# Kernel optimization log

Hardware: AMD Instinct MI355X
Metric: run time of the kernel (lower is better)

## Reference

```python
import jax, jax.numpy as jnp
import numpy as np

LN_EPS = 1e-5  # torch nn.LayerNorm default


def setup_inputs() -> dict:
    key = jax.random.key(0)
    ks = jax.random.split(key, 5)
    B, N, K, H, D = 1, 16384, 16, 4, 32
    q = jax.random.normal(ks[0], (B, N, H, D), dtype=jnp.float32)
    k_neigh = jax.random.normal(ks[1], (B, N, K, H, D), dtype=jnp.float32)
    v_neigh = jax.random.normal(ks[2], (B, N, K, H, D), dtype=jnp.float32)
    geo_f = jax.random.normal(ks[3], (B, N, K, D), dtype=jnp.float32)
    W = jax.random.normal(ks[4], (D, D), dtype=jnp.float32) * (1.0 / np.sqrt(D))
    b = jnp.zeros((D,), dtype=jnp.float32)
    ln_gamma = jnp.ones((D,), dtype=jnp.float32)
    ln_beta = jnp.zeros((D,), dtype=jnp.float32)
    return {"q": q, "k_neigh": k_neigh, "v_neigh": v_neigh, "geo_f": geo_f,
            "W": W, "b": b, "ln_gamma": ln_gamma, "ln_beta": ln_beta}


def reference(q, k_neigh, v_neigh, geo_f, W, b, ln_gamma, ln_beta):
    # q: [B,N,H,D], k_neigh/v_neigh: [B,N,K,H,D], geo_f: [B,N,K,D]
    scale = q.shape[-1] ** (-0.5)
    # broadcasted edge tensor [B,N,K,H,D]
    w = (q[:, :, None, :, :] - k_neigh + geo_f[:, :, :, None, :]) / scale
    # Linear(hdim,hdim) + ReLU + LayerNorm(hdim)
    w = jnp.einsum('bnkhd,ed->bnkhe', w, W) + b
    w = jax.nn.relu(w)
    mu = jnp.mean(w, axis=-1, keepdims=True)
    var = jnp.mean(jnp.square(w - mu), axis=-1, keepdims=True)
    w = (w - mu) * jax.lax.rsqrt(var + LN_EPS) * ln_gamma + ln_beta
    # subtract detached per-neighbor max (shift-invariant for softmax)
    w = w - jax.lax.stop_gradient(jnp.max(w, axis=2, keepdims=True))
    attn = jax.nn.softmax(w, axis=2)  # softmax over K neighbors
    # dropout p=0.0 -> identity
    out = jnp.sum(attn * v_neigh, axis=2)  # [B,N,H,D]
    return out
```

## Files before the change

kernel.cpp:

```cpp
#include <hip/hip_runtime.h>
#include <math.h>

constexpr int KNB = 16;
constexpr int HH  = 4;
constexpr int DD  = 32;

typedef __attribute__((ext_vector_type(4))) float f32x4;
typedef __attribute__((ext_vector_type(8))) short bf16x8;
typedef __attribute__((ext_vector_type(4))) short s16x4;

__device__ __forceinline__ unsigned short f2bf(float f) {
    union { float f; unsigned u; } v; v.f = f;
    const unsigned r = v.u + 0x7fffu + ((v.u >> 16) & 1u);
    return (unsigned short)(r >> 16);
}
__device__ __forceinline__ float bf2f(unsigned short b) {
    union { unsigned u; float f; } v; v.u = ((unsigned)b) << 16; return v.f;
}

__global__ __launch_bounds__(256) void geoneigh_mfma(
    const float* __restrict__ q, const float* __restrict__ kn,
    const float* __restrict__ vn, const float* __restrict__ geo,
    const float* __restrict__ W, const float* __restrict__ bvec,
    const float* __restrict__ gamma, const float* __restrict__ beta,
    float* __restrict__ out, int BN)
{
    __shared__ short wt[4][2][2][16][32];

    const int l  = threadIdx.x & 63;
    const int wv = threadIdx.x >> 6;
    const int gw = blockIdx.x * 4 + wv;
    const int n  = gw >> 1;
    if (n >= BN) return;
    const int h0 = (gw & 1) * 2;

    const int lm = l & 15;
    const int lg = l >> 4;
    const int r8 = l >> 3;
    const int dq = l & 7;

    bf16x8 Wh[2], Wl[2];
    #pragma unroll
    for (int t = 0; t < 2; ++t) {
        const float* wr = &W[(t * 16 + lm) * DD + lg * 8];
        const float4 a = *(const float4*)wr;
        const float4 b = *(const float4*)(wr + 4);
        const float wf[8] = {a.x, a.y, a.z, a.w, b.x, b.y, b.z, b.w};
        #pragma unroll
        for (int j = 0; j < 8; ++j) {
            const unsigned short h = f2bf(wf[j]);
            Wh[t][j] = (short)h;
            Wl[t][j] = (short)f2bf(wf[j] - bf2f(h));
        }
    }
    float bias[2], gam[2], bet[2];
    #pragma unroll
    for (int t = 0; t < 2; ++t) {
        bias[t] = bvec[lm + 16 * t];
        gam[t]  = gamma[lm + 16 * t];
        bet[t]  = beta[lm + 16 * t];
    }

    const float SC = 5.656854249492381f;

    float4 g4[2], q4[2], k4[2][2];
    #pragma unroll
    for (int j = 0; j < 2; ++j)
        g4[j] = *(const float4*)&geo[((size_t)n * KNB + r8 + 8 * j) * DD + dq * 4];
    #pragma unroll
    for (int u = 0; u < 2; ++u) {
        const int h = h0 + u;
        q4[u] = *(const float4*)&q[((size_t)n * HH + h) * DD + dq * 4];
        #pragma unroll
        for (int j = 0; j < 2; ++j)
            k4[u][j] = *(const float4*)&kn[(((size_t)n * KNB + r8 + 8 * j) * HH + h) * DD + dq * 4];
    }

    #pragma unroll
    for (int u = 0; u < 2; ++u) {
        #pragma unroll
        for (int j = 0; j < 2; ++j) {
            const int row = r8 + 8 * j;
            const float w0 = (q4[u].x - k4[u][j].x + g4[j].x) * SC;
            const float w1 = (q4[u].y - k4[u][j].y + g4[j].y) * SC;
            const float w2 = (q4[u].z - k4[u][j].z + g4[j].z) * SC;
            const float w3 = (q4[u].w - k4[u][j].w + g4[j].w) * SC;
            const unsigned short a0 = f2bf(w0), a1 = f2bf(w1), a2 = f2bf(w2), a3 = f2bf(w3);
            const s16x4 hi = {(short)a0, (short)a1, (short)a2, (short)a3};
            const s16x4 lo = {(short)f2bf(w0 - bf2f(a0)), (short)f2bf(w1 - bf2f(a1)),
                              (short)f2bf(w2 - bf2f(a2)), (short)f2bf(w3 - bf2f(a3))};
            *(s16x4*)&wt[wv][u][0][row][dq * 4] = hi;
            *(s16x4*)&wt[wv][u][1][row][dq * 4] = lo;
        }
    }
    asm volatile("" ::: "memory");

    bf16x8 Ah[2], Al[2];
    #pragma unroll
    for (int u = 0; u < 2; ++u) {
        Ah[u] = *(const bf16x8*)&wt[wv][u][0][lm][lg * 8];
        Al[u] = *(const bf16x8*)&wt[wv][u][1][lm][lg * 8];
    }

    float vreg[2][2][4];
    #pragma unroll
    for (int u = 0; u < 2; ++u)
        #pragma unroll
        for (int t = 0; t < 2; ++t)
            #pragma unroll
            for (int r = 0; r < 4; ++r)
                vreg[u][t][r] =
                    vn[(((size_t)n * KNB + lg * 4 + r) * HH + h0 + u) * DD + lm + 16 * t];

    f32x4 acc[2][2];
    #pragma unroll
    for (int u = 0; u < 2; ++u)
        #pragma unroll
        for (int t = 0; t < 2; ++t) {
            f32x4 c = {0.f, 0.f, 0.f, 0.f};
            c = __builtin_amdgcn_mfma_f32_16x16x32_bf16(Ah[u], Wh[t], c, 0, 0, 0);
            c = __builtin_amdgcn_mfma_f32_16x16x32_bf16(Ah[u], Wl[t], c, 0, 0, 0);
            c = __builtin_amdgcn_mfma_f32_16x16x32_bf16(Al[u], Wh[t], c, 0, 0, 0);
            acc[u][t] = c;
        }

    #pragma unroll
    for (int u = 0; u < 2; ++u) {
        float x[2][4], t1[4], t2[4];
        #pragma unroll
        for (int t = 0; t < 2; ++t)
            #pragma unroll
            for (int r = 0; r < 4; ++r)
                x[t][r] = fmaxf(acc[u][t][r] + bias[t], 0.f);
        #pragma unroll
        for (int r = 0; r < 4; ++r) {
            t1[r] = x[0][r] + x[1][r];
            t2[r] = x[0][r] * x[0][r] + x[1][r] * x[1][r];
        }
        #pragma unroll
        for (int m = 1; m <= 8; m <<= 1) {
            #pragma unroll
            for (int r = 0; r < 4; ++r) {
                t1[r] += __shfl_xor(t1[r], m);
                t2[r] += __shfl_xor(t2[r], m);
            }
        }
        float z[2][4];
        #pragma unroll
        for (int r = 0; r < 4; ++r) {
            const float mu  = t1[r] * 0.03125f;
            const float var = fmaxf(t2[r] * 0.03125f - mu * mu, 0.f);
            const float inv = rsqrtf(var + 1e-5f);
            #pragma unroll
            for (int t = 0; t < 2; ++t)
                z[t][r] = (x[t][r] - mu) * inv * gam[t] + bet[t];
        }
        float S[2], o[2];
        #pragma unroll
        for (int t = 0; t < 2; ++t) {
            float mx = fmaxf(fmaxf(z[t][0], z[t][1]), fmaxf(z[t][2], z[t][3]));
            mx = fmaxf(mx, __shfl_xor(mx, 16));
            mx = fmaxf(mx, __shfl_xor(mx, 32));
            float s = 0.f, oo = 0.f;
            #pragma unroll
            for (int r = 0; r < 4; ++r) {
                const float p = __expf(z[t][r] - mx);
                s += p;
                oo = fmaf(p, vreg[u][t][r], oo);
            }
            s  += __shfl_xor(s, 16);
            s  += __shfl_xor(s, 32);
            oo += __shfl_xor(oo, 16);
            oo += __shfl_xor(oo, 32);
            S[t] = s; o[t] = oo;
        }
        if (l < 32) {
            const int   sel = lg & 1;
            const float os  = sel ? o[1] : o[0];
            const float ss  = sel ? S[1] : S[0];
            out[((size_t)n * HH + h0 + u) * DD + l] = __fdividef(os, ss);
        }
    }
}

extern "C" void kernel_launch(void* const* d_in, const int* in_sizes, int n_in,
                              void* d_out, int out_size, void* d_ws, size_t ws_size,
                              hipStream_t stream) {
    const float* q   = (const float*)d_in[0];
    const float* kn  = (const float*)d_in[1];
    const float* vn  = (const float*)d_in[2];
    const float* geo = (const float*)d_in[3];
    const float* W   = (const float*)d_in[4];
    const float* b   = (const float*)d_in[5];
    const float* gam = (const float*)d_in[6];
    const float* bet = (const float*)d_in[7];
    float* out = (float*)d_out;

    const int BN     = in_sizes[0] / (HH * DD);
    const int waves  = BN * 2;
    const int blocks = (waves + 3) / 4;

    hipLaunchKernelGGL(geoneigh_mfma, dim3(blocks), dim3(256), 0, stream,
                       q, kn, vn, geo, W, b, gam, bet, out, BN);
}
```

Measured before the change: 66.90 us.

## Load MFMA A-fragments directly from global memory, skipping the LDS staging

Each lane now loads q, k and geo in the exact layout of the MFMA A-operand (row = neighbor, 8 contiguous d values). This removes the shared-memory write/read round trip used before to transpose the edge tensor. It also folds the 1/scale factor into W, seeds the accumulator with the bias, uses packed hardware bf16 conversions, and merges the two per-head output stores into one full-wave store. The direct loads are 32-byte per lane with a different coalescing pattern, and each q row is now read by 16 lanes.

```diff
diff --git a/kernel.cpp b/kernel.cpp
--- a/kernel.cpp
+++ b/kernel.cpp
@@ -1,4 +1,5 @@
 #include <hip/hip_runtime.h>
+#include <hip/hip_bf16.h>
 #include <math.h>
 
 constexpr int KNB = 16;
@@ -7,50 +8,51 @@
 
 typedef __attribute__((ext_vector_type(4))) float f32x4;
 typedef __attribute__((ext_vector_type(8))) short bf16x8;
-typedef __attribute__((ext_vector_type(4))) short s16x4;
-
-__device__ __forceinline__ unsigned short f2bf(float f) {
-    union { float f; unsigned u; } v; v.f = f;
-    const unsigned r = v.u + 0x7fffu + ((v.u >> 16) & 1u);
-    return (unsigned short)(r >> 16);
-}
-__device__ __forceinline__ float bf2f(unsigned short b) {
-    union { unsigned u; float f; } v; v.u = ((unsigned)b) << 16; return v.f;
-}
-
-__global__ __launch_bounds__(256) void geoneigh_mfma(
+
+union BFRAG { bf16x8 v; unsigned u[4]; };
+
+__device__ __forceinline__ unsigned pk_bf16(float a, float b) {
+    union { __hip_bfloat162 b2; unsigned u; } r;
+    r.b2 = __float22bfloat162_rn(make_float2(a, b));
+    return r.u;
+}
+__device__ __forceinline__ float2 unpk_bf16(unsigned u) {
+    union { unsigned u; __hip_bfloat162 b2; } r; r.u = u;
+    return make_float2(__bfloat162float(r.b2.x), __bfloat162float(r.b2.y));
+}
+
+__global__ __launch_bounds__(256) void geoneigh_mfma2(
     const float* __restrict__ q, const float* __restrict__ kn,
     const float* __restrict__ vn, const float* __restrict__ geo,
     const float* __restrict__ W, const float* __restrict__ bvec,
     const float* __restrict__ gamma, const float* __restrict__ beta,
     float* __restrict__ out, int BN)
 {
-    __shared__ short wt[4][2][2][16][32];
-
     const int l  = threadIdx.x & 63;
-    const int wv = threadIdx.x >> 6;
-    const int gw = blockIdx.x * 4 + wv;
+    const int gw = blockIdx.x * 4 + (threadIdx.x >> 6);
     const int n  = gw >> 1;
     if (n >= BN) return;
     const int h0 = (gw & 1) * 2;
 
     const int lm = l & 15;
     const int lg = l >> 4;
-    const int r8 = l >> 3;
-    const int dq = l & 7;
-
-    bf16x8 Wh[2], Wl[2];
+
+    const float SC = 5.656854249492381f;
+
+    BFRAG Wh[2], Wl[2];
     #pragma unroll
     for (int t = 0; t < 2; ++t) {
         const float* wr = &W[(t * 16 + lm) * DD + lg * 8];
-        const float4 a = *(const float4*)wr;
-        const float4 b = *(const float4*)(wr + 4);
-        const float wf[8] = {a.x, a.y, a.z, a.w, b.x, b.y, b.z, b.w};
-        #pragma unroll
-        for (int j = 0; j < 8; ++j) {
-            const unsigned short h = f2bf(wf[j]);
-            Wh[t][j] = (short)h;
-            Wl[t][j] = (short)f2bf(wf[j] - bf2f(h));
+        const float4 wa = *(const float4*)wr;
+        const float4 wb = *(const float4*)(wr + 4);
+        float wf[8] = {wa.x * SC, wa.y * SC, wa.z * SC, wa.w * SC,
+                       wb.x * SC, wb.y * SC, wb.z * SC, wb.w * SC};
+        #pragma unroll
+        for (int p = 0; p < 4; ++p) {
+            const unsigned h = pk_bf16(wf[2 * p], wf[2 * p + 1]);
+            const float2 hr = unpk_bf16(h);
+            Wh[t].u[p] = h;
+            Wl[t].u[p] = pk_bf16(wf[2 * p] - hr.x, wf[2 * p + 1] - hr.y);
         }
     }
     float bias[2], gam[2], bet[2];
@@ -61,69 +63,64 @@
         bet[t]  = beta[lm + 16 * t];
     }
 
-    const float SC = 5.656854249492381f;
-
-    float4 g4[2], q4[2], k4[2][2];
-    #pragma unroll
-    for (int j = 0; j < 2; ++j)
-        g4[j] = *(const float4*)&geo[((size_t)n * KNB + r8 + 8 * j) * DD + dq * 4];
+    const size_t nn = (size_t)n;
+    const float* kb = kn  + ((nn * KNB + lm) * HH + h0) * DD + lg * 8;
+    const float* gb = geo + (nn * KNB + lm) * DD + lg * 8;
+    const float* qb = q   + (nn * HH + h0) * DD + lg * 8;
+
+    const float4 gf0 = *(const float4*)gb;
+    const float4 gf1 = *(const float4*)(gb + 4);
+    float4 kf[2][2], qf[2][2];
     #pragma unroll
     for (int u = 0; u < 2; ++u) {
-        const int h = h0 + u;
-        q4[u] = *(const float4*)&q[((size_t)n * HH + h) * DD + dq * 4];
-        #pragma unroll
-        for (int j = 0; j < 2; ++j)
-            k4[u][j] = *(const float4*)&kn[(((size_t)n * KNB + r8 + 8 * j) * HH + h) * DD + dq * 4];
-    }
-
+        kf[u][0] = *(const float4*)(kb + u * DD);
+        kf[u][1] = *(const float4*)(kb + u * DD + 4);
+        qf[u][0] = *(const float4*)(qb + u * DD);
+        qf[u][1] = *(const float4*)(qb + u * DD + 4);
+    }
+
+    const float* vb = vn + ((nn * KNB + lg * 4) * HH + h0) * DD + lm;
+    float vreg[2][2][4];
+    #pragma unroll
+    for (int u = 0; u < 2; ++u)
+        #pragma unroll
+        for (int t = 0; t < 2; ++t)
+            #pragma unroll
+            for (int r = 0; r < 4; ++r)
+                vreg[u][t][r] = vb[((size_t)r * HH + u) * DD + 16 * t];
+
+    f32x4 acc[2][2];
     #pragma unroll
     for (int u = 0; u < 2; ++u) {
-        #pragma unroll
-        for (int j = 0; j < 2; ++j) {
-            const int row = r8 + 8 * j;
-            const float w0 = (q4[u].x - k4[u][j].x + g4[j].x) * SC;
-            const float w1 = (q4[u].y - k4[u][j].y + g4[j].y) * SC;
-            const float w2 = (q4[u].z - k4[u][j].z + g4[j].z) * SC;
-            const float w3 = (q4[u].w - k4[u][j].w + g4[j].w) * SC;
-            const unsigned short a0 = f2bf(w0), a1 = f2bf(w1), a2 = f2bf(w2), a3 = f2bf(w3);
-            const s16x4 hi = {(short)a0, (short)a1, (short)a2, (short)a3};
-            const s16x4 lo = {(short)f2bf(w0 - bf2f(a0)), (short)f2bf(w1 - bf2f(a1)),
-                              (short)f2bf(w2 - bf2f(a2)), (short)f2bf(w3 - bf2f(a3))};
-            *(s16x4*)&wt[wv][u][0][row][dq * 4] = hi;
-            *(s16x4*)&wt[wv][u][1][row][dq * 4] = lo;
-        }
-    }
-    asm volatile("" ::: "memory");
-
-    bf16x8 Ah[2], Al[2];
-    #pragma unroll
-    for (int u = 0; u < 2; ++u) {
-        Ah[u] = *(const bf16x8*)&wt[wv][u][0][lm][lg * 8];
-        Al[u] = *(const bf16x8*)&wt[wv][u][1][lm][lg * 8];
-    }
-
-    float vreg[2][2][4];
-    #pragma unroll
-    for (int u = 0; u < 2; ++u)
-        #pragma unroll
-        for (int t = 0; t < 2; ++t)
-            #pragma unroll
-            for (int r = 0; r < 4; ++r)
-                vreg[u][t][r] =
-                    vn[(((size_t)n * KNB + lg * 4 + r) * HH + h0 + u) * DD + lm + 16 * t];
-
-    f32x4 acc[2][2];
-    #pragma unroll
-    for (int u = 0; u < 2; ++u)
+        float wv[8];
+        #pragma unroll
+        for (int p = 0; p < 2; ++p) {
+            const float4 kq = kf[u][p], qq = qf[u][p];
+            const float4 gg = p ? gf1 : gf0;
+            wv[4 * p + 0] = qq.x - kq.x + gg.x;
+            wv[4 * p + 1] = qq.y - kq.y + gg.y;
+            wv[4 * p + 2] = qq.z - kq.z + gg.z;
+            wv[4 * p + 3] = qq.w - kq.w + gg.w;
+        }
+        BFRAG Ah, Al;
+        #pragma unroll
+        for (int p = 0; p < 4; ++p) {
+            const unsigned h = pk_bf16(wv[2 * p], wv[2 * p + 1]);
+            const float2 hr = unpk_bf16(h);
+            Ah.u[p] = h;
+            Al.u[p] = pk_bf16(wv[2 * p] - hr.x, wv[2 * p + 1] - hr.y);
+        }
         #pragma unroll
         for (int t = 0; t < 2; ++t) {
-            f32x4 c = {0.f, 0.f, 0.f, 0.f};
-            c = __builtin_amdgcn_mfma_f32_16x16x32_bf16(Ah[u], Wh[t], c, 0, 0, 0);
-            c = __builtin_amdgcn_mfma_f32_16x16x32_bf16(Ah[u], Wl[t], c, 0, 0, 0);
-            c = __builtin_amdgcn_mfma_f32_16x16x32_bf16(Al[u], Wh[t], c, 0, 0, 0);
+            f32x4 c = {bias[t], bias[t], bias[t], bias[t]};
+            c = __builtin_amdgcn_mfma_f32_16x16x32_bf16(Ah.v, Wh[t].v, c, 0, 0, 0);
+            c = __builtin_amdgcn_mfma_f32_16x16x32_bf16(Ah.v, Wl[t].v, c, 0, 0, 0);
+            c = __builtin_amdgcn_mfma_f32_16x16x32_bf16(Al.v, Wh[t].v, c, 0, 0, 0);
             acc[u][t] = c;
         }
-
+    }
+
+    float outv[2], sumv[2];
     #pragma unroll
     for (int u = 0; u < 2; ++u) {
         float x[2][4], t1[4], t2[4];
@@ -131,7 +128,7 @@
         for (int t = 0; t < 2; ++t)
             #pragma unroll
             for (int r = 0; r < 4; ++r)
-                x[t][r] = fmaxf(acc[u][t][r] + bias[t], 0.f);
+                x[t][r] = fmaxf(acc[u][t][r], 0.f);
         #pragma unroll
         for (int r = 0; r < 4; ++r) {
             t1[r] = x[0][r] + x[1][r];
@@ -174,13 +171,15 @@
             oo += __shfl_xor(oo, 32);
             S[t] = s; o[t] = oo;
         }
-        if (l < 32) {
-            const int   sel = lg & 1;
-            const float os  = sel ? o[1] : o[0];
-            const float ss  = sel ? S[1] : S[0];
-            out[((size_t)n * HH + h0 + u) * DD + l] = __fdividef(os, ss);
-        }
-    }
+        const int sel = lg & 1;
+        outv[u] = sel ? o[1] : o[0];
+        sumv[u] = sel ? S[1] : S[0];
+    }
+
+    const int us = l >> 5;
+    const float oo = us ? outv[1] : outv[0];
+    const float ss = us ? sumv[1] : sumv[0];
+    out[(nn * HH + h0 + us) * DD + (l & 31)] = __fdividef(oo, ss);
 }
 
 extern "C" void kernel_launch(void* const* d_in, const int* in_sizes, int n_in,
@@ -200,6 +199,6 @@
     const int waves  = BN * 2;
     const int blocks = (waves + 3) / 4;
 
-    hipLaunchKernelGGL(geoneigh_mfma, dim3(blocks), dim3(256), 0, stream,
+    hipLaunchKernelGGL(geoneigh_mfma2, dim3(blocks), dim3(256), 0, stream,
                        q, kn, vn, geo, W, b, gam, bet, out, BN);
 }
```

New measurement: 72.42 us. +8.3%, slower.
